# Optimization experiments

Measured on AMD Instinct MI355X. Metric: run time of the kernel, lower is better.

The kernel has to match this reference:

```python
import jax, jax.numpy as jnp
import numpy as np

N_NODES = 20000
N_EDGES = 256000
N_GRAPHS = 512
F_IN = 75
HEADS = 10
OUT_DIM = 128
NEG_SLOPE = 0.2


def _gat_conv(x, src, dst, W, a_src, a_dst, bias, n_nodes):
    # PyG GATConv (v1 style): h = x W per head; e_ij = LeakyReLU(a_src.h_i + a_dst.h_j)
    # softmax over edges sharing the same destination, then scatter-sum messages.
    H, F = a_src.shape
    h = (x @ W).reshape(n_nodes, H, F)                      # [N, H, F]
    alpha_src = jnp.einsum('nhf,hf->nh', h, a_src)          # [N, H]
    alpha_dst = jnp.einsum('nhf,hf->nh', h, a_dst)          # [N, H]
    e = alpha_src[src] + alpha_dst[dst]                     # [E, H]
    e = jax.nn.leaky_relu(e, NEG_SLOPE)
    emax = jax.ops.segment_max(e, dst, num_segments=n_nodes)
    ee = jnp.exp(e - emax[dst])
    denom = jax.ops.segment_sum(ee, dst, num_segments=n_nodes)
    alpha = ee / (denom[dst] + 1e-16)                       # [E, H]
    msg = h[src] * alpha[:, :, None]                        # [E, H, F]
    out = jax.ops.segment_sum(msg, dst, num_segments=n_nodes)
    return out.reshape(n_nodes, H * F) + bias


def setup_inputs() -> dict:
    key = jax.random.key(0)
    ks = jax.random.split(key, 12)
    x = jax.random.normal(ks[0], (N_NODES, F_IN), dtype=jnp.float32)
    edge_index = jax.random.randint(ks[1], (2, N_EDGES), 0, N_NODES, dtype=jnp.int32)
    batch = jnp.sort(jax.random.randint(ks[2], (N_NODES,), 0, N_GRAPHS, dtype=jnp.int32))
    s = 0.05
    return {
        'x': x, 'edge_index': edge_index, 'batch': batch,
        'W1': jax.random.normal(ks[3], (F_IN, HEADS * F_IN), dtype=jnp.float32) * s,
        'a_src1': jax.random.normal(ks[4], (HEADS, F_IN), dtype=jnp.float32) * s,
        'a_dst1': jax.random.normal(ks[5], (HEADS, F_IN), dtype=jnp.float32) * s,
        'b1': jnp.zeros((HEADS * F_IN,), dtype=jnp.float32),
        'W2': jax.random.normal(ks[6], (HEADS * F_IN, OUT_DIM), dtype=jnp.float32) * s,
        'a_src2': jax.random.normal(ks[7], (1, OUT_DIM), dtype=jnp.float32) * s,
        'a_dst2': jax.random.normal(ks[8], (1, OUT_DIM), dtype=jnp.float32) * s,
        'b2': jnp.zeros((OUT_DIM,), dtype=jnp.float32),
        'Wg': jax.random.normal(ks[9], (OUT_DIM, OUT_DIM), dtype=jnp.float32) * s,
        'bg': jnp.zeros((OUT_DIM,), dtype=jnp.float32),
    }


def reference(x, edge_index, batch, W1, a_src1, a_dst1, b1, W2, a_src2, a_dst2, b2, Wg, bg):
    n = x.shape[0]
    # PyG GATConv adds self-loops by default
    loops = jnp.arange(n, dtype=edge_index.dtype)
    src = jnp.concatenate([edge_index[0], loops])
    dst = jnp.concatenate([edge_index[1], loops])
    # dropout layers are identity in eval mode
    h = jax.nn.elu(_gat_conv(x, src, dst, W1, a_src1, a_dst1, b1, n))      # [N, 750]
    h = jax.nn.relu(_gat_conv(h, src, dst, W2, a_src2, a_dst2, b2, n))     # [N, 128]
    # global max pool per graph
    g = jax.ops.segment_max(h, batch, num_segments=N_GRAPHS)
    g = jnp.where(jnp.isfinite(g), g, 0.0)  # empty graphs -> 0
    return jax.nn.relu(g @ Wg + bg)                                         # [G, 128]
```

## Files before the change

### kernel.cpp

```cpp
#include <hip/hip_runtime.h>
#include <hip/hip_bf16.h>
#include <math.h>

#define N_NODES  20000
#define N_EDGES  256000
#define E_TOT    276000
#define N_GRAPHS 512
#define F_IN     75
#define HEADS    10
#define D1       750
#define XK       80
#define XKP      96
#define HOUT     80
#define D2P      800
#define OUT_DIM  128
#define NPAD     20096
#define CAP      96

typedef __attribute__((ext_vector_type(8))) short bf16x8;
typedef __attribute__((ext_vector_type(8))) unsigned short u16x8;
typedef __attribute__((ext_vector_type(4))) float f32x4;

__device__ __forceinline__ unsigned short f2bf(float v) {
    unsigned int u = __float_as_uint(v);
    u += 0x7fffu + ((u >> 16) & 1u);
    return (unsigned short)(u >> 16);
}
__device__ __forceinline__ float bf2f(unsigned short u) {
    return __uint_as_float(((unsigned int)u) << 16);
}

#define PS1 (20*F_IN)
#define PS2 (PS1 + N_NODES*XK)
#define PS3 (PS2 + HEADS*HOUT*XKP)
#define PS4 (PS3 + OUT_DIM*D2P)
#define PS5 (PS4 + N_NODES)
#define PS6 (PS5 + N_GRAPHS*OUT_DIM)

__global__ __launch_bounds__(256) void k_prep(const float* __restrict__ x,
                                              const float* __restrict__ W1,
                                              const float* __restrict__ a_s,
                                              const float* __restrict__ a_d,
                                              const float* __restrict__ W2,
                                              float* __restrict__ va,
                                              unsigned short* __restrict__ xbp,
                                              unsigned short* __restrict__ w1bh,
                                              unsigned short* __restrict__ w2t,
                                              int* __restrict__ cnt,
                                              float* __restrict__ g) {
    int id = blockIdx.x*256 + threadIdx.x;
    if (id < PS1) {
        int p = id / F_IN, k = id - p*F_IN;
        int h = (p < HEADS) ? p : p - HEADS;
        const float* avec = (p < HEADS) ? (a_s + h*F_IN) : (a_d + h*F_IN);
        float s = 0.f;
        for (int f=0; f<F_IN; f++) s += avec[f] * W1[(size_t)k*D1 + h*F_IN + f];
        va[id] = s;
    } else if (id < PS2) {
        int i = id - PS1;
        int r = i / XK, c = i - r*XK;
        xbp[i] = (c < F_IN) ? f2bf(x[(size_t)r*F_IN + c]) : 0;
    } else if (id < PS3) {
        int i = id - PS2;
        int h = i / (HOUT*XKP);
        int r = i - h*(HOUT*XKP);
        int j = r / XKP, k = r - j*XKP;
        w1bh[i] = (j < F_IN && k < F_IN) ? f2bf(W1[(size_t)k*D1 + h*F_IN + j]) : 0;
    } else if (id < PS4) {
        int i = id - PS3;
        int j = i / D2P, c = i - j*D2P;
        int h = c / HOUT, kk = c - h*HOUT;
        w2t[i] = (kk < F_IN) ? f2bf(W2[(size_t)(h*F_IN+kk)*OUT_DIM + j]) : 0;
    } else if (id < PS5) {
        cnt[id - PS4] = 0;
    } else if (id < PS6) {
        g[id - PS5] = 0.f;
    }
}

#define SCAT_BLOCKS ((E_TOT+255)/256)
#define ALPHA_BLOCKS ((N_NODES*20+255)/256)
__global__ __launch_bounds__(256) void k_scat_alpha(const int* __restrict__ ei,
                                                    int* __restrict__ cnt, int* __restrict__ bucket,
                                                    const float* __restrict__ x, const float* __restrict__ va,
                                                    float* __restrict__ aso, float* __restrict__ ado) {
    if (blockIdx.x < SCAT_BLOCKS) {
        int e = blockIdx.x*256 + threadIdx.x;
        if (e >= E_TOT) return;
        int s, d;
        if (e < N_EDGES) { s = ei[e]; d = ei[N_EDGES+e]; }
        else             { s = e - N_EDGES; d = s; }
        int pos = atomicAdd(&cnt[d], 1);
        if (pos < CAP) bucket[(size_t)d*CAP + pos] = s;
    } else {
        int at = ((int)blockIdx.x - SCAT_BLOCKS)*256 + (int)threadIdx.x;
        if (at >= N_NODES*20) return;
        int n = at / 20, p = at - n*20;
        const float* xr = x  + (size_t)n*F_IN;
        const float* vr = va + p*F_IN;
        float s = 0.f;
        #pragma unroll 5
        for (int k=0;k<F_IN;k++) s += xr[k]*vr[k];
        if (p < HEADS) aso[n*HEADS + p] = s;
        else           ado[n*HEADS + (p-HEADS)] = s;
    }
}

#define CH1 24
__global__ __launch_bounds__(128) void k_fagg1(const unsigned short* __restrict__ xbp,
                                               const float* __restrict__ aso,
                                               const float* __restrict__ ado,
                                               const int* __restrict__ cnt,
                                               const int* __restrict__ bucket,
                                               unsigned short* __restrict__ xaggb) {
    int n = blockIdx.x, t = threadIdx.x;
    __shared__ float els[CH1][HEADS];
    int deg = min(cnt[n], CAP);
    const int* brow = bucket + (size_t)n*CAP;
    if (t >= 100 && t < 120) {
        int hh = (t-100) >> 1, half = (t-100) & 1;
        *(u16x8*)(xaggb + (size_t)n*960 + hh*XKP + XK + half*8) = (u16x8){0,0,0,0,0,0,0,0};
    }
    const int h1 = t % 10, u1 = t / 10;
    const float adn1 = (t < 120) ? ado[(size_t)n*HEADS + h1] : 0.f;
    const int h2 = t / 10, k8 = (t - h2*10) * 8;
    float acc[8] = {0,0,0,0,0,0,0,0};
    float den = 0.f;

    for (int base = 0; base < deg; base += CH1) {
        int m = min(CH1, deg - base);
        if (t < 120) {
            if (u1 < m) {
                int src = brow[base + u1];
                float v = aso[(size_t)src*HEADS + h1] + adn1;
                v = v > 0.f ? v : 0.2f*v;
                els[u1][h1] = __expf(v);
            }
            int u2 = u1 + 12;
            if (u2 < m) {
                int src = brow[base + u2];
                float v = aso[(size_t)src*HEADS + h1] + adn1;
                v = v > 0.f ? v : 0.2f*v;
                els[u2][h1] = __expf(v);
            }
        }
        __syncthreads();
        if (t < 100) {
            int u = 0;
            for (; u + 4 <= m; u += 4) {
                int sA = brow[base+u], sB = brow[base+u+1], sC = brow[base+u+2], sD = brow[base+u+3];
                float eA = els[u][h2], eB = els[u+1][h2], eC = els[u+2][h2], eD = els[u+3][h2];
                u16x8 xA = *(const u16x8*)(xbp + (size_t)sA*XK + k8);
                u16x8 xB = *(const u16x8*)(xbp + (size_t)sB*XK + k8);
                u16x8 xC = *(const u16x8*)(xbp + (size_t)sC*XK + k8);
                u16x8 xD = *(const u16x8*)(xbp + (size_t)sD*XK + k8);
                den += eA + eB + eC + eD;
                #pragma unroll
                for (int c=0;c<8;c++)
                    acc[c] += bf2f(xA[c])*eA + bf2f(xB[c])*eB + bf2f(xC[c])*eC + bf2f(xD[c])*eD;
            }
            for (; u < m; u++) {
                int src = brow[base+u];
                float e = els[u][h2];
                den += e;
                u16x8 xv = *(const u16x8*)(xbp + (size_t)src*XK + k8);
                #pragma unroll
                for (int c=0;c<8;c++) acc[c] += bf2f(xv[c]) * e;
            }
        }
        __syncthreads();
    }
    if (t < 100) {
        float iv = 1.f / (den + 1e-16f);
        u16x8 ov;
        #pragma unroll
        for (int c=0;c<8;c++) ov[c] = f2bf(acc[c] * iv);
        *(u16x8*)(xaggb + (size_t)n*960 + h2*XKP + k8) = ov;
    }
}


#define GLD16(g, s) __builtin_amdgcn_global_load_lds( \
    (const __attribute__((address_space(1))) void*)(g), \
    (__attribute__((address_space(3))) void*)(s), 16, 0, 0)

__global__ __launch_bounds__(256) void k_gemmh(const unsigned short* __restrict__ A,
                                               const unsigned short* __restrict__ B,
                                               const float* __restrict__ b1,
                                               unsigned short* __restrict__ h1act) {
    __shared__ char lds[2][9216];
    const int t = threadIdx.x, l = t & 63, w = t >> 6;
    const int n0 = blockIdx.x * 64;
    const int h  = blockIdx.y;
    const unsigned short* Ah = A + (size_t)h*XKP;
    const unsigned short* Bh = B + (size_t)h*HOUT*XKP;

    const int arow  = t >> 2;
    const int aslot = (t & 3) ^ ((t >> 3) & 3);

    f32x4 acc[5];
    #pragma unroll
    for (int n=0;n<5;n++) acc[n] = (f32x4){0.f,0.f,0.f,0.f};

    auto stage = [&](int ks, int buf) {
        const int k0 = ks * 32;
        GLD16(Ah + (size_t)(n0 + arow)*960 + k0 + aslot*8, lds[buf] + t*16);
        GLD16(Bh + (size_t)arow*XKP        + k0 + aslot*8, lds[buf] + 4096 + t*16);
        if (t < 64)
            GLD16(Bh + (size_t)(64 + arow)*XKP + k0 + aslot*8, lds[buf] + 8192 + t*16);
    };

    const int fr = l & 15;
    const int fs = ((l >> 4) ^ ((fr >> 1) & 3));
    const int abyte = (w*16 + fr)*64 + fs*16;

    stage(0, 0);
    int cb = 0;
    for (int ks = 0; ks < 3; ks++) {
        __syncthreads();
        if (ks + 1 < 3) stage(ks+1, cb^1);
        const char* Ab = lds[cb];
        const char* Bb = lds[cb] + 4096;
        bf16x8 af = *(const bf16x8*)(Ab + abyte);
        bf16x8 bfr[5];
        #pragma unroll
        for (int n=0;n<5;n++) bfr[n] = *(const bf16x8*)(Bb + (n*16 + fr)*64 + fs*16);
        #pragma unroll
        for (int n=0;n<5;n++)
            acc[n] = __builtin_amdgcn_mfma_f32_16x16x32_bf16(af, bfr[n], acc[n], 0, 0, 0);
        cb ^= 1;
    }

    const int rbase = n0 + w*16 + (l>>4)*4;
    #pragma unroll
    for (int n=0;n<5;n++) {
        int jp = n*16 + (l & 15);
        #pragma unroll
        for (int q=0;q<4;q++) {
            int node = rbase + q;
            unsigned short r = 0;
            if (jp < F_IN) {
                float v = acc[n][q] + b1[h*F_IN + jp];
                r = f2bf(v > 0.f ? v : __expf(v) - 1.f);
            }
            h1act[(size_t)node*D2P + h*HOUT + jp] = r;
        }
    }
}

__global__ __launch_bounds__(256) void k_gemm2m(const unsigned short* __restrict__ A,
                                                const unsigned short* __restrict__ Bt,
                                                const float* __restrict__ a_s2,
                                                const float* __restrict__ a_d2,
                                                unsigned short* __restrict__ C,
                                                float* __restrict__ aso2,
                                                float* __restrict__ ado2) {
    __shared__ char lds[2][12288];
    __shared__ float sm_ps[64], sm_pd[64];
    const int t  = threadIdx.x;
    const int l  = t & 63;
    const int w  = t >> 6;
    const int wr = w >> 1, wc = w & 1;
    const int n0 = blockIdx.x * 64;

    const int arow  = t >> 2;
    const int aslot = (t & 3) ^ ((t >> 3) & 3);
    const int brow1 = arow + 64;

    f32x4 acc[2][4];
    #pragma unroll
    for (int m=0;m<2;m++)
        #pragma unroll
        for (int n=0;n<4;n++) acc[m][n] = (f32x4){0.f,0.f,0.f,0.f};

    auto stage = [&](int ks, int buf) {
        const int k0 = ks * 32;
        GLD16(A  + (size_t)(n0 + arow)*D2P + k0 + aslot*8, lds[buf] + t*16);
        GLD16(Bt + (size_t)arow       *D2P + k0 + aslot*8, lds[buf] + 4096 + t*16);
        GLD16(Bt + (size_t)brow1      *D2P + k0 + aslot*8, lds[buf] + 8192 + t*16);
    };

    const int fr   = l & 15;
    const int fs   = ((l >> 4) ^ ((fr >> 1) & 3));
    const int abyte = (wr*32 + fr)*64 + fs*16;
    const int bbyte = (wc*64 + fr)*64 + fs*16;

    stage(0, 0);
    int cb = 0;
    for (int ks = 0; ks < D2P/32; ks++) {
        __syncthreads();
        if (ks+1 < D2P/32) stage(ks+1, cb^1);
        const char* Ab = lds[cb];
        const char* Bb = lds[cb] + 4096;
        bf16x8 af[2], bfr[4];
        #pragma unroll
        for (int m=0;m<2;m++) af[m] = *(const bf16x8*)(Ab + abyte + m*1024);
        #pragma unroll
        for (int n=0;n<4;n++) bfr[n] = *(const bf16x8*)(Bb + bbyte + n*1024);
        #pragma unroll
        for (int m=0;m<2;m++)
            #pragma unroll
            for (int n=0;n<4;n++)
                acc[m][n] = __builtin_amdgcn_mfma_f32_16x16x32_bf16(af[m], bfr[n], acc[m][n], 0, 0, 0);
        cb ^= 1;
    }

    #pragma unroll
    for (int m=0;m<2;m++) {
        int rbase = n0 + wr*32 + m*16 + (l>>4)*4;
        #pragma unroll
        for (int n=0;n<4;n++) {
            int col = wc*64 + n*16 + (l&15);
            #pragma unroll
            for (int q=0;q<4;q++) {
                int node = rbase + q;
                if (node < N_NODES) C[(size_t)node*OUT_DIM + col] = f2bf(acc[m][n][q]);
            }
        }
    }

    float av[4], bv[4];
    #pragma unroll
    for (int n=0;n<4;n++) {
        int col = wc*64 + n*16 + (l&15);
        av[n] = a_s2[col];
        bv[n] = a_d2[col];
    }
    float psv[8], pdv[8];
    #pragma unroll
    for (int m=0;m<2;m++) {
        #pragma unroll
        for (int q=0;q<4;q++) {
            float ps = 0.f, pd = 0.f;
            #pragma unroll
            for (int n=0;n<4;n++) { ps += acc[m][n][q]*av[n]; pd += acc[m][n][q]*bv[n]; }
            #pragma unroll
            for (int o=8;o;o>>=1) { ps += __shfl_xor(ps,o); pd += __shfl_xor(pd,o); }
            psv[m*4+q] = ps; pdv[m*4+q] = pd;
            if (wc == 0 && (l&15) == 0) {
                int r = wr*32 + m*16 + (l>>4)*4 + q;
                sm_ps[r] = ps; sm_pd[r] = pd;
            }
        }
    }
    __syncthreads();
    if (wc == 1 && (l&15) == 0) {
        #pragma unroll
        for (int m=0;m<2;m++) {
            #pragma unroll
            for (int q=0;q<4;q++) {
                int r = wr*32 + m*16 + (l>>4)*4 + q;
                int node = n0 + r;
                if (node < N_NODES) {
                    aso2[node] = sm_ps[r] + psv[m*4+q];
                    ado2[node] = sm_pd[r] + pdv[m*4+q];
                }
            }
        }
    }
}

#define CH2 32
__global__ __launch_bounds__(128) void k_fagg2(const unsigned short* __restrict__ h2b,
                                               const float* __restrict__ aso,
                                               const float* __restrict__ ado,
                                               const int* __restrict__ cnt,
                                               const int* __restrict__ bucket,
                                               const float* __restrict__ b2,
                                               const int* __restrict__ batch,
                                               float* __restrict__ g) {
    int n = blockIdx.x, j = threadIdx.x;
    __shared__ float els[CH2];
    __shared__ int   srcl[CH2];
    int deg = min(cnt[n], CAP);
    const int* brow = bucket + (size_t)n*CAP;
    float adn = ado[n];
    float acc = 0.f, den = 0.f;
    for (int base = 0; base < deg; base += CH2) {
        int m = min(CH2, deg - base);
        if (j < m) {
            int sv = brow[base + j];
            srcl[j] = sv;
            float v = aso[sv] + adn;
            v = v > 0.f ? v : 0.2f*v;
            els[j] = __expf(v);
        }
        __syncthreads();
        int u = 0;
        for (; u + 8 <= m; u += 8) {
            float e[8], hv[8];
            #pragma unroll
            for (int q=0;q<8;q++) { e[q] = els[u+q]; }
            #pragma unroll
            for (int q=0;q<8;q++) { hv[q] = bf2f(h2b[(size_t)srcl[u+q]*OUT_DIM + j]); }
            #pragma unroll
            for (int q=0;q<8;q++) { den += e[q]; acc += hv[q]*e[q]; }
        }
        for (; u < m; u++) {
            float e = els[u];
            den += e;
            acc += bf2f(h2b[(size_t)srcl[u]*OUT_DIM + j]) * e;
        }
        __syncthreads();
    }
    float v = acc / (den + 1e-16f) + b2[j];
    v = v > 0.f ? v : 0.f;
    atomicMax((int*)&g[(size_t)batch[n]*OUT_DIM + j], __float_as_int(v));
}

__global__ __launch_bounds__(128) void k_final(const float* __restrict__ g, const float* __restrict__ Wg,
                                               const float* __restrict__ bg, float* __restrict__ out) {
    __shared__ float gl[128];
    int gr = blockIdx.x, j = threadIdx.x;
    gl[j] = g[gr*OUT_DIM + j];
    __syncthreads();
    float acc = 0.f;
    for (int k=0;k<OUT_DIM;k++) acc += gl[k]*Wg[k*OUT_DIM + j];
    float v = acc + bg[j];
    out[gr*OUT_DIM + j] = v>0.f ? v : 0.f;
}


extern "C" void kernel_launch(void* const* d_in, const int* in_sizes, int n_in,
                              void* d_out, int out_size, void* d_ws, size_t ws_size,
                              hipStream_t stream) {
    const float* x     = (const float*)d_in[0];
    const int*   ei    = (const int*)d_in[1];
    const int*   batch = (const int*)d_in[2];
    const float* W1    = (const float*)d_in[3];
    const float* as1   = (const float*)d_in[4];
    const float* ad1   = (const float*)d_in[5];
    const float* b1    = (const float*)d_in[6];
    const float* W2    = (const float*)d_in[7];
    const float* as2   = (const float*)d_in[8];
    const float* ad2   = (const float*)d_in[9];
    const float* b2    = (const float*)d_in[10];
    const float* Wg    = (const float*)d_in[11];
    const float* bg    = (const float*)d_in[12];
    float* out = (float*)d_out;

    char* ws = (char*)d_ws;
    size_t o = 0;
    auto alloc = [&](size_t bytes) { char* p = ws + o; o = (o + bytes + 255) & ~(size_t)255; return p; };
    unsigned short* xaggb  = (unsigned short*)alloc((size_t)NPAD*960*2);
    unsigned short* h1act  = (unsigned short*)alloc((size_t)NPAD*D2P*2);
    unsigned short* xbp    = (unsigned short*)alloc((size_t)N_NODES*XK*2);
    unsigned short* w1bh   = (unsigned short*)alloc((size_t)HEADS*HOUT*XKP*2);
    unsigned short* w2t    = (unsigned short*)alloc((size_t)OUT_DIM*D2P*2);
    float*          va     = (float*)alloc((size_t)20*F_IN*4);
    float*          aso1   = (float*)alloc((size_t)N_NODES*HEADS*4);
    float*          ado1   = (float*)alloc((size_t)N_NODES*HEADS*4);
    float*          aso2   = (float*)alloc((size_t)N_NODES*4);
    float*          ado2   = (float*)alloc((size_t)N_NODES*4);
    int*            cnt    = (int*)alloc((size_t)N_NODES*4);
    int*            bucket = (int*)alloc((size_t)N_NODES*CAP*4);
    float*          g      = (float*)alloc((size_t)N_GRAPHS*OUT_DIM*4);
    unsigned short* h2b    = (unsigned short*)xaggb;

    k_prep      <<<(PS6+255)/256, 256, 0, stream>>>(x, W1, as1, ad1, W2, va, xbp, w1bh, w2t, cnt, g);
    k_scat_alpha<<<SCAT_BLOCKS + ALPHA_BLOCKS, 256, 0, stream>>>(ei, cnt, bucket, x, va, aso1, ado1);
    k_fagg1     <<<N_NODES, 128, 0, stream>>>(xbp, aso1, ado1, cnt, bucket, xaggb);
    k_gemmh     <<<dim3(NPAD/64, HEADS), 256, 0, stream>>>(xaggb, w1bh, b1, h1act);
    k_gemm2m    <<<NPAD/64, 256, 0, stream>>>(h1act, w2t, as2, ad2, h2b, aso2, ado2);
    k_fagg2     <<<N_NODES, 128, 0, stream>>>(h2b, aso2, ado2, cnt, bucket, b2, batch, g);
    k_final     <<<N_GRAPHS, 128, 0, stream>>>(g, Wg, bg, out);
}
```

Before: 217.1 us.

## Map one wavefront per node in layer-2 aggregation with shuffles and paired loads

Reworks the second GAT aggregation kernel so each 64-lane wavefront handles one destination node, with four nodes per 256-thread block. Each lane loads two bf16 features at once. Neighbour indices and attention weights are broadcast with warp shuffles instead of shared memory, which removes the block barriers. The intent is to cut launch granularity, synchronisation and load-instruction count. In exchange, each lane issues twice as many atomicMax operations and sums in a different order.

```diff
diff --git a/kernel.cpp b/kernel.cpp
--- a/kernel.cpp
+++ b/kernel.cpp
@@ -360,8 +360,7 @@
     }
 }
 
-#define CH2 32
-__global__ __launch_bounds__(128) void k_fagg2(const unsigned short* __restrict__ h2b,
+__global__ __launch_bounds__(256) void k_fagg2(const unsigned short* __restrict__ h2b,
                                                const float* __restrict__ aso,
                                                const float* __restrict__ ado,
                                                const int* __restrict__ cnt,
@@ -369,43 +368,54 @@
                                                const float* __restrict__ b2,
                                                const int* __restrict__ batch,
                                                float* __restrict__ g) {
-    int n = blockIdx.x, j = threadIdx.x;
-    __shared__ float els[CH2];
-    __shared__ int   srcl[CH2];
+    int n    = blockIdx.x*4 + (threadIdx.x >> 6);
+    int lane = threadIdx.x & 63;
+    if (n >= N_NODES) return;
     int deg = min(cnt[n], CAP);
     const int* brow = bucket + (size_t)n*CAP;
     float adn = ado[n];
-    float acc = 0.f, den = 0.f;
-    for (int base = 0; base < deg; base += CH2) {
-        int m = min(CH2, deg - base);
-        if (j < m) {
-            int sv = brow[base + j];
-            srcl[j] = sv;
+    const int j2 = lane*2;
+    float acc0 = 0.f, acc1 = 0.f, den = 0.f;
+
+    for (int base = 0; base < deg; base += 64) {
+        int m = min(64, deg - base);
+        int   sv = 0;
+        float ev = 0.f;
+        if (lane < m) {
+            sv = brow[base + lane];
             float v = aso[sv] + adn;
             v = v > 0.f ? v : 0.2f*v;
-            els[j] = __expf(v);
-        }
-        __syncthreads();
+            ev = __expf(v);
+        }
         int u = 0;
-        for (; u + 8 <= m; u += 8) {
-            float e[8], hv[8];
-            #pragma unroll
-            for (int q=0;q<8;q++) { e[q] = els[u+q]; }
-            #pragma unroll
-            for (int q=0;q<8;q++) { hv[q] = bf2f(h2b[(size_t)srcl[u+q]*OUT_DIM + j]); }
-            #pragma unroll
-            for (int q=0;q<8;q++) { den += e[q]; acc += hv[q]*e[q]; }
+        for (; u + 4 <= m; u += 4) {
+            int   sA = __shfl(sv, u),   sB = __shfl(sv, u+1),   sC = __shfl(sv, u+2),   sD = __shfl(sv, u+3);
+            float eA = __shfl(ev, u),   eB = __shfl(ev, u+1),   eC = __shfl(ev, u+2),   eD = __shfl(ev, u+3);
+            ushort2 hA = *(const ushort2*)(h2b + (size_t)sA*OUT_DIM + j2);
+            ushort2 hB = *(const ushort2*)(h2b + (size_t)sB*OUT_DIM + j2);
+            ushort2 hC = *(const ushort2*)(h2b + (size_t)sC*OUT_DIM + j2);
+            ushort2 hD = *(const ushort2*)(h2b + (size_t)sD*OUT_DIM + j2);
+            den  += eA + eB + eC + eD;
+            acc0 += bf2f(hA.x)*eA + bf2f(hB.x)*eB + bf2f(hC.x)*eC + bf2f(hD.x)*eD;
+            acc1 += bf2f(hA.y)*eA + bf2f(hB.y)*eB + bf2f(hC.y)*eC + bf2f(hD.y)*eD;
         }
         for (; u < m; u++) {
-            float e = els[u];
-            den += e;
-            acc += bf2f(h2b[(size_t)srcl[u]*OUT_DIM + j]) * e;
-        }
-        __syncthreads();
-    }
-    float v = acc / (den + 1e-16f) + b2[j];
-    v = v > 0.f ? v : 0.f;
-    atomicMax((int*)&g[(size_t)batch[n]*OUT_DIM + j], __float_as_int(v));
+            int   s = __shfl(sv, u);
+            float e = __shfl(ev, u);
+            ushort2 hv = *(const ushort2*)(h2b + (size_t)s*OUT_DIM + j2);
+            den  += e;
+            acc0 += bf2f(hv.x)*e;
+            acc1 += bf2f(hv.y)*e;
+        }
+    }
+    float iv = 1.f / (den + 1e-16f);
+    float v0 = acc0*iv + b2[j2];
+    float v1 = acc1*iv + b2[j2+1];
+    v0 = v0 > 0.f ? v0 : 0.f;
+    v1 = v1 > 0.f ? v1 : 0.f;
+    float* grow = g + (size_t)batch[n]*OUT_DIM;
+    atomicMax((int*)&grow[j2],   __float_as_int(v0));
+    atomicMax((int*)&grow[j2+1], __float_as_int(v1));
 }
 
 __global__ __launch_bounds__(128) void k_final(const float* __restrict__ g, const float* __restrict__ Wg,
@@ -462,6 +472,6 @@
     k_fagg1     <<<N_NODES, 128, 0, stream>>>(xbp, aso1, ado1, cnt, bucket, xaggb);
     k_gemmh     <<<dim3(NPAD/64, HEADS), 256, 0, stream>>>(xaggb, w1bh, b1, h1act);
     k_gemm2m    <<<NPAD/64, 256, 0, stream>>>(h1act, w2t, as2, ad2, h2b, aso2, ado2);
-    k_fagg2     <<<N_NODES, 128, 0, stream>>>(h2b, aso2, ado2, cnt, bucket, b2, batch, g);
+    k_fagg2     <<<(N_NODES+3)/4, 256, 0, stream>>>(h2b, aso2, ado2, cnt, bucket, b2, batch, g);
     k_final     <<<N_GRAPHS, 128, 0, stream>>>(g, Wg, bg, out);
 }
```

After: 217.7 us. Within noise of the previous version (+0.3%).
